# Kernel tuning notes

Measured on AMD Instinct MI355X. Metric: run time of the kernel, lower is better.

The kernel has to match this reference:

```python
import jax, jax.numpy as jnp
import numpy as np

FP8_MAX = 448.0  # max normal for float8_e4m3fn
BLOCK = 128


def setup_inputs() -> dict:
    key = jax.random.key(0)
    k1, k2, k3 = jax.random.split(key, 3)
    B, S, D_IN, D_OUT = 2, 2048, 4096, 8192
    x = jax.random.normal(k1, (B, S, D_IN), dtype=jnp.float32)
    # stored weight is fp8_e4m3fn; materialize as f32 values that are exactly fp8-representable
    w = jax.random.normal(k2, (D_OUT, D_IN), dtype=jnp.float32)
    weight = w.astype(jnp.float8_e4m3fn).astype(jnp.float32)
    # positive per-(128x128)-block dequant scales
    weight_scale_inv = (
        jax.random.uniform(k3, (D_OUT // BLOCK, D_IN // BLOCK), dtype=jnp.float32) * 0.05 + 0.005
    )
    return {"x": x, "weight": weight, "weight_scale_inv": weight_scale_inv}


def _quantize_per_token(x2d):
    # x2d: [M, K] -> fp8 values + [M, 1] f32 scale
    amax = jnp.clip(jnp.max(jnp.abs(x2d), axis=-1, keepdims=True), min=1e-12)
    x_scale = (amax / FP8_MAX).astype(jnp.float32)
    x_fp8 = (x2d / x_scale).astype(jnp.float8_e4m3fn)
    return x_fp8, x_scale


def _dequantize_weight(weight, weight_scale_inv):
    # weight: [O, K] (fp8-representable f32), scales: [O/B, K/B]
    O, K = weight.shape
    w_fp8 = weight.astype(jnp.float8_e4m3fn).astype(jnp.float32)
    wb = w_fp8.reshape(O // BLOCK, BLOCK, K // BLOCK, BLOCK)
    wb = wb * weight_scale_inv[:, None, :, None]
    return wb.reshape(O, K)


def reference(x, weight, weight_scale_inv):
    orig_shape = x.shape
    x2d = x.reshape(-1, orig_shape[-1])  # [M, K], M > 1 path
    x_fp8, x_scale = _quantize_per_token(x2d)
    # block-scaled fp8 GEMM: y[m,n] = x_scale[m] * sum_k x_fp8[m,k] * w_fp8[n,k] * s[n//B,k//B]
    w_deq = _dequantize_weight(weight, weight_scale_inv)  # [O, K]
    y = jnp.einsum("mk,ok->mo", x_fp8.astype(jnp.float32), w_deq) * x_scale
    return y.reshape(*orig_shape[:-1], weight.shape[0])
```

## Files before the change

### kernel.cpp

```cpp
#include <hip/hip_runtime.h>

typedef float f32x4  __attribute__((ext_vector_type(4)));
typedef float f32x16 __attribute__((ext_vector_type(16)));
typedef int   i32x4  __attribute__((ext_vector_type(4)));
typedef int   i32x8  __attribute__((ext_vector_type(8)));

#define AS1 __attribute__((address_space(1)))
#define AS3 __attribute__((address_space(3)))

__global__ __launch_bounds__(256) void quant_x_fp8_kernel(
    const float* __restrict__ x, unsigned char* __restrict__ x8,
    float* __restrict__ xs, int K) {
  int m = blockIdx.x;
  int t = threadIdx.x;
  const f32x4* src = (const f32x4*)(x + (size_t)m * K + t * 16);
  f32x4 v[4];
  float am = 0.0f;
#pragma unroll
  for (int i = 0; i < 4; ++i) {
    v[i] = src[i];
#pragma unroll
    for (int j = 0; j < 4; ++j) am = fmaxf(am, __builtin_fabsf(v[i][j]));
  }
#pragma unroll
  for (int off = 32; off >= 1; off >>= 1)
    am = fmaxf(am, __shfl_xor(am, off, 64));
  __shared__ float red[4];
  int wv = t >> 6, lane = t & 63;
  if (lane == 0) red[wv] = am;
  __syncthreads();
  am = fmaxf(fmaxf(red[0], red[1]), fmaxf(red[2], red[3]));
  am = fmaxf(am, 1e-12f);
  float sc = am / 448.0f;
  if (t == 0) xs[m] = sc;
  i32x4 out;
#pragma unroll
  for (int i = 0; i < 4; ++i) {
    float q0 = v[i][0] / sc, q1 = v[i][1] / sc;
    float q2 = v[i][2] / sc, q3 = v[i][3] / sc;
    int p = __builtin_amdgcn_cvt_pk_fp8_f32(q0, q1, 0, false);
    p = __builtin_amdgcn_cvt_pk_fp8_f32(q2, q3, p, true);
    out[i] = p;
  }
  *(i32x4*)(x8 + (size_t)m * K + t * 16) = out;
}

__global__ __launch_bounds__(256) void quant_w_fp8_kernel(
    const float* __restrict__ w, unsigned char* __restrict__ w8) {
  size_t idx = (size_t)blockIdx.x * 256 + threadIdx.x;
  const f32x4* src = (const f32x4*)w + idx * 4;
  i32x4 out;
#pragma unroll
  for (int i = 0; i < 4; ++i) {
    f32x4 v = src[i];
    int p = __builtin_amdgcn_cvt_pk_fp8_f32(v[0], v[1], 0, false);
    p = __builtin_amdgcn_cvt_pk_fp8_f32(v[2], v[3], p, true);
    out[i] = p;
  }
  ((i32x4*)w8)[idx] = out;
}

__global__ __launch_bounds__(256, 2) void gemm_mxfp8_kernel(
    const unsigned char* __restrict__ A8,
    const unsigned char* __restrict__ W8,
    const float* __restrict__ xs,
    const float* __restrict__ wsinv,
    float* __restrict__ Y,
    int M, int N, int K) {
  const int KB = K >> 7;

  int bid = blockIdx.x, nwg = gridDim.x;
  int wg = (bid & 7) * (nwg >> 3) + (bid >> 3);
  int mt = M >> 7;
  int bm = wg & (mt - 1);
  int bn = wg / mt;
  int m0 = bm << 7, n0 = bn << 7;

  __shared__ __align__(16) char lds[65536];

  const int tid = threadIdx.x, wv = tid >> 6, lane = tid & 63;
  const int wr = wv >> 1, wc = wv & 1;
  const int l31 = lane & 31, hi2 = lane >> 5;
  const int salt = l31 & 7;

  const int sL0 = ((hi2 * 2 + 0) ^ salt) << 4;
  const int sH0 = ((hi2 * 2 + 1) ^ salt) << 4;
  const int sL1 = ((4 + hi2 * 2 + 0) ^ salt) << 4;
  const int sH1 = ((4 + hi2 * 2 + 1) ^ salt) << 4;

  const int aRow = (wr * 64 + l31) * 128;
  const int bRow = (wc * 64 + l31) * 128;
  const int aL0 = aRow + sL0, aH0 = aRow + sH0;
  const int aL1 = aRow + sL1, aH1 = aRow + sH1;
  const int bL0 = bRow + sL0, bH0 = bRow + sH0;
  const int bL1 = bRow + sL1, bH1 = bRow + sH1;

  const int stgD = tid << 4;
  const int rIdx = tid >> 3;
  const int cSrc = ((tid & 7) ^ ((tid >> 3) & 7)) << 4;
  const size_t rowB = (size_t)K;
  const size_t g32 = 32 * rowB;
  const char* pA = (const char*)A8 + (size_t)(m0 + rIdx) * rowB + cSrc;
  const char* pB = (const char*)W8 + (size_t)(n0 + rIdx) * rowB + cSrc;

  const float* wsv = wsinv + (size_t)bn * KB;

  f32x16 acc[2][2];
#pragma unroll
  for (int i = 0; i < 2; ++i)
#pragma unroll
    for (int j = 0; j < 2; ++j) acc[i][j] = (f32x16)0.0f;

  i32x8 af[2], bf[2][2];

#define GL(SRC, DST)                                                           \
  __builtin_amdgcn_global_load_lds((const AS1 void*)(SRC), (AS3 void*)(DST),   \
                                   16, 0, 0)
#define STG(COND, SB, SRC)                                                     \
  if (COND) {                                                                  \
    const char* s_ = (SRC);                                                    \
    char* d_ = lds + (SB) + stgD;                                              \
    GL(s_, d_);                                                                \
    GL(s_ + g32, d_ + 4096);                                                   \
    GL(s_ + 2 * g32, d_ + 8192);                                               \
    GL(s_ + 3 * g32, d_ + 12288);                                              \
  }

#define RD_A(RB, MJ)                                                           \
  {                                                                            \
    const char* p_ = lds + (RB) + (MJ) * 4096;                                 \
    i32x4 lo0 = *(const i32x4*)(p_ + aL0);                                     \
    i32x4 hi0 = *(const i32x4*)(p_ + aH0);                                     \
    i32x4 lo1 = *(const i32x4*)(p_ + aL1);                                     \
    i32x4 hi1 = *(const i32x4*)(p_ + aH1);                                     \
    af[0] = __builtin_shufflevector(lo0, hi0, 0, 1, 2, 3, 4, 5, 6, 7);         \
    af[1] = __builtin_shufflevector(lo1, hi1, 0, 1, 2, 3, 4, 5, 6, 7);         \
  }
#define RD_B(RB)                                                               \
  _Pragma("unroll") for (int nj = 0; nj < 2; ++nj) {                           \
    const char* p_ = lds + (RB) + 16384 + nj * 4096;                           \
    i32x4 lo0 = *(const i32x4*)(p_ + bL0);                                     \
    i32x4 hi0 = *(const i32x4*)(p_ + bH0);                                     \
    i32x4 lo1 = *(const i32x4*)(p_ + bL1);                                     \
    i32x4 hi1 = *(const i32x4*)(p_ + bH1);                                     \
    bf[nj][0] = __builtin_shufflevector(lo0, hi0, 0, 1, 2, 3, 4, 5, 6, 7);     \
    bf[nj][1] = __builtin_shufflevector(lo1, hi1, 0, 1, 2, 3, 4, 5, 6, 7);     \
  }

#define MMFn(MJ, NJ, R_)                                                       \
  {                                                                            \
    _Pragma("unroll") for (int q = 0; q < 16; ++q)                             \
        acc[MJ][NJ][q] *= (R_);                                                \
    acc[MJ][NJ] = __builtin_amdgcn_mfma_scale_f32_32x32x64_f8f6f4(             \
        af[0], bf[NJ][0], acc[MJ][NJ], 0, 0, 0, 0x7f7f7f7f, 0, 0x7f7f7f7f);    \
    acc[MJ][NJ] = __builtin_amdgcn_mfma_scale_f32_32x32x64_f8f6f4(             \
        af[1], bf[NJ][1], acc[MJ][NJ], 0, 0, 0, 0x7f7f7f7f, 0, 0x7f7f7f7f);    \
  }

  STG(true, 0, pA);
  STG(true, 16384, pB);
  asm volatile("s_waitcnt vmcnt(0)" ::: "memory");
  __builtin_amdgcn_s_barrier();

  const char* pAs = pA + 128;
  const char* pBs = pB + 128;
  float sp_ = wsv[0];

#define TILE(T, RB, SB, G)                                                     \
  {                                                                            \
    float sc_ = wsv[(T)];                                                      \
    float r_ = sp_ / sc_;                                                      \
    RD_B(RB);                                                                  \
    RD_A(RB, 0);                                                               \
    STG(G, (SB), pAs);                                                         \
    STG(G, (SB) + 16384, pBs);                                                 \
    __builtin_amdgcn_s_setprio(1);                                             \
    MMFn(0, 0, r_);                                                            \
    MMFn(0, 1, r_);                                                            \
    __builtin_amdgcn_s_setprio(0);                                             \
    RD_A(RB, 1);                                                               \
    __builtin_amdgcn_s_setprio(1);                                             \
    MMFn(1, 0, r_);                                                            \
    MMFn(1, 1, r_);                                                            \
    __builtin_amdgcn_s_setprio(0);                                             \
    sp_ = sc_;                                                                 \
    asm volatile("s_waitcnt vmcnt(0)" ::: "memory");                           \
    __builtin_amdgcn_s_barrier();                                              \
    pAs += 128;                                                                \
    pBs += 128;                                                                \
  }

#pragma unroll 1
  for (int t = 0; t < KB; t += 2) {
    TILE(t, 0, 32768, true)
    TILE(t + 1, 32768, 0, (t + 2) < KB)
  }

#undef TILE
#undef MMFn
#undef RD_B
#undef RD_A
#undef STG
#undef GL

  const float sl_ = sp_;
#pragma unroll
  for (int mj = 0; mj < 2; ++mj)
#pragma unroll
    for (int nj = 0; nj < 2; ++nj) {
      int col = n0 + wc * 64 + nj * 32 + l31;
#pragma unroll
      for (int q = 0; q < 4; ++q) {
        int row0 = m0 + wr * 64 + mj * 32 + q * 8 + hi2 * 4;
        f32x4 sv = *(const f32x4*)(xs + row0);
#pragma unroll
        for (int j = 0; j < 4; ++j)
          Y[(size_t)(row0 + j) * N + col] = acc[mj][nj][q * 4 + j] * sv[j] * sl_;
      }
    }
}

extern "C" void kernel_launch(void* const* d_in, const int* in_sizes, int n_in,
                              void* d_out, int out_size, void* d_ws, size_t ws_size,
                              hipStream_t stream) {
  const float* x     = (const float*)d_in[0];
  const float* w     = (const float*)d_in[1];
  const float* wsinv = (const float*)d_in[2];
  float* y = (float*)d_out;

  const int K = 4096;
  const int M = in_sizes[0] / K;
  const int N = in_sizes[1] / K;

  unsigned char* x8 = (unsigned char*)d_ws;
  float* xs = (float*)((char*)d_ws + (size_t)M * K);
  unsigned char* w8 =
      (unsigned char*)d_ws + (size_t)M * K + (size_t)M * 4;

  quant_x_fp8_kernel<<<M, 256, 0, stream>>>(x, x8, xs, K);
  quant_w_fp8_kernel<<<(int)(((size_t)N * K / 16 + 255) / 256), 256, 0,
                       stream>>>(w, w8);

  dim3 grid((M / 128) * (N / 128));
  gemm_mxfp8_kernel<<<grid, 256, 0, stream>>>(x8, w8, xs, wsinv, y, M, N, K);
}
```

Before: 219.6 us.

## Load weight fragments directly from global into registers, bypassing LDS

B (weight) operands are no longer staged through LDS. Each lane loads its own MFMA fragments from global memory straight into registers, double-buffered across tiles (even/odd register sets). LDS shrinks to 32 KB, holding only the A tiles, which cuts LDS traffic and may allow more workgroups per CU. In exchange, weight data is no longer shared between waves with the same column (wr duplicates), so global/L2 traffic for B rises, register pressure goes up, and the per-lane loads are less coalesced.

After: 349.8 us. 1.59x slower.

```diff
diff --git a/kernel.cpp b/kernel.cpp
--- a/kernel.cpp
+++ b/kernel.cpp
@@ -76,7 +76,7 @@
   int bn = wg / mt;
   int m0 = bm << 7, n0 = bn << 7;
 
-  __shared__ __align__(16) char lds[65536];
+  __shared__ __align__(16) char lds[32768];
 
   const int tid = threadIdx.x, wv = tid >> 6, lane = tid & 63;
   const int wr = wv >> 1, wc = wv & 1;
@@ -89,19 +89,19 @@
   const int sH1 = ((4 + hi2 * 2 + 1) ^ salt) << 4;
 
   const int aRow = (wr * 64 + l31) * 128;
-  const int bRow = (wc * 64 + l31) * 128;
   const int aL0 = aRow + sL0, aH0 = aRow + sH0;
   const int aL1 = aRow + sL1, aH1 = aRow + sH1;
-  const int bL0 = bRow + sL0, bH0 = bRow + sH0;
-  const int bL1 = bRow + sL1, bH1 = bRow + sH1;
 
   const int stgD = tid << 4;
   const int rIdx = tid >> 3;
-  const int cSrc = ((tid & 7) ^ ((tid >> 3) & 7)) << 4;
+  const int cSrc = ((tid & 7) ^ (rIdx & 7)) << 4;
   const size_t rowB = (size_t)K;
   const size_t g32 = 32 * rowB;
   const char* pA = (const char*)A8 + (size_t)(m0 + rIdx) * rowB + cSrc;
-  const char* pB = (const char*)W8 + (size_t)(n0 + rIdx) * rowB + cSrc;
+
+  const char* pB0 = (const char*)W8 + (size_t)(n0 + wc * 64 + l31) * rowB +
+                    hi2 * 32;
+  const char* pB1 = pB0 + 32 * rowB;
 
   const float* wsv = wsinv + (size_t)bn * KB;
 
@@ -111,12 +111,12 @@
 #pragma unroll
     for (int j = 0; j < 2; ++j) acc[i][j] = (f32x16)0.0f;
 
-  i32x8 af[2], bf[2][2];
+  i32x8 af[2], bfE[2][2], bfO[2][2];
 
 #define GL(SRC, DST)                                                           \
   __builtin_amdgcn_global_load_lds((const AS1 void*)(SRC), (AS3 void*)(DST),   \
                                    16, 0, 0)
-#define STG(COND, SB, SRC)                                                     \
+#define STG_A(COND, SB, SRC)                                                   \
   if (COND) {                                                                  \
     const char* s_ = (SRC);                                                    \
     char* d_ = lds + (SB) + stgD;                                              \
@@ -136,71 +136,78 @@
     af[0] = __builtin_shufflevector(lo0, hi0, 0, 1, 2, 3, 4, 5, 6, 7);         \
     af[1] = __builtin_shufflevector(lo1, hi1, 0, 1, 2, 3, 4, 5, 6, 7);         \
   }
-#define RD_B(RB)                                                               \
-  _Pragma("unroll") for (int nj = 0; nj < 2; ++nj) {                           \
-    const char* p_ = lds + (RB) + 16384 + nj * 4096;                           \
-    i32x4 lo0 = *(const i32x4*)(p_ + bL0);                                     \
-    i32x4 hi0 = *(const i32x4*)(p_ + bH0);                                     \
-    i32x4 lo1 = *(const i32x4*)(p_ + bL1);                                     \
-    i32x4 hi1 = *(const i32x4*)(p_ + bH1);                                     \
-    bf[nj][0] = __builtin_shufflevector(lo0, hi0, 0, 1, 2, 3, 4, 5, 6, 7);     \
-    bf[nj][1] = __builtin_shufflevector(lo1, hi1, 0, 1, 2, 3, 4, 5, 6, 7);     \
-  }
-
-#define MMFn(MJ, NJ, R_)                                                       \
+
+#define LDB(COND, DST)                                                         \
+  if (COND) {                                                                  \
+    i32x4 l0 = *(const i32x4*)(pB0);                                           \
+    i32x4 h0 = *(const i32x4*)(pB0 + 16);                                      \
+    i32x4 l1 = *(const i32x4*)(pB0 + 64);                                      \
+    i32x4 h1 = *(const i32x4*)(pB0 + 80);                                      \
+    DST[0][0] = __builtin_shufflevector(l0, h0, 0, 1, 2, 3, 4, 5, 6, 7);       \
+    DST[0][1] = __builtin_shufflevector(l1, h1, 0, 1, 2, 3, 4, 5, 6, 7);       \
+    l0 = *(const i32x4*)(pB1);                                                 \
+    h0 = *(const i32x4*)(pB1 + 16);                                            \
+    l1 = *(const i32x4*)(pB1 + 64);                                            \
+    h1 = *(const i32x4*)(pB1 + 80);                                            \
+    DST[1][0] = __builtin_shufflevector(l0, h0, 0, 1, 2, 3, 4, 5, 6, 7);       \
+    DST[1][1] = __builtin_shufflevector(l1, h1, 0, 1, 2, 3, 4, 5, 6, 7);       \
+  }
+
+#define MMFn(MJ, NJ, R_, BF)                                                   \
   {                                                                            \
     _Pragma("unroll") for (int q = 0; q < 16; ++q)                             \
         acc[MJ][NJ][q] *= (R_);                                                \
     acc[MJ][NJ] = __builtin_amdgcn_mfma_scale_f32_32x32x64_f8f6f4(             \
-        af[0], bf[NJ][0], acc[MJ][NJ], 0, 0, 0, 0x7f7f7f7f, 0, 0x7f7f7f7f);    \
+        af[0], BF[NJ][0], acc[MJ][NJ], 0, 0, 0, 0x7f7f7f7f, 0, 0x7f7f7f7f);    \
     acc[MJ][NJ] = __builtin_amdgcn_mfma_scale_f32_32x32x64_f8f6f4(             \
-        af[1], bf[NJ][1], acc[MJ][NJ], 0, 0, 0, 0x7f7f7f7f, 0, 0x7f7f7f7f);    \
-  }
-
-  STG(true, 0, pA);
-  STG(true, 16384, pB);
+        af[1], BF[NJ][1], acc[MJ][NJ], 0, 0, 0, 0x7f7f7f7f, 0, 0x7f7f7f7f);    \
+  }
+
+  STG_A(true, 0, pA);
+  LDB(true, bfE);
+  pB0 += 128;
+  pB1 += 128;
   asm volatile("s_waitcnt vmcnt(0)" ::: "memory");
   __builtin_amdgcn_s_barrier();
 
   const char* pAs = pA + 128;
-  const char* pBs = pB + 128;
   float sp_ = wsv[0];
 
-#define TILE(T, RB, SB, G)                                                     \
+#define TILE(T, RB, SB, G, BFC, BFN)                                           \
   {                                                                            \
     float sc_ = wsv[(T)];                                                      \
     float r_ = sp_ / sc_;                                                      \
-    RD_B(RB);                                                                  \
+    sp_ = sc_;                                                                 \
+    LDB(G, BFN);                                                               \
+    STG_A(G, (SB), pAs);                                                       \
     RD_A(RB, 0);                                                               \
-    STG(G, (SB), pAs);                                                         \
-    STG(G, (SB) + 16384, pBs);                                                 \
     __builtin_amdgcn_s_setprio(1);                                             \
-    MMFn(0, 0, r_);                                                            \
-    MMFn(0, 1, r_);                                                            \
+    MMFn(0, 0, r_, BFC);                                                       \
+    MMFn(0, 1, r_, BFC);                                                       \
     __builtin_amdgcn_s_setprio(0);                                             \
     RD_A(RB, 1);                                                               \
     __builtin_amdgcn_s_setprio(1);                                             \
-    MMFn(1, 0, r_);                                                            \
-    MMFn(1, 1, r_);                                                            \
+    MMFn(1, 0, r_, BFC);                                                       \
+    MMFn(1, 1, r_, BFC);                                                       \
     __builtin_amdgcn_s_setprio(0);                                             \
-    sp_ = sc_;                                                                 \
     asm volatile("s_waitcnt vmcnt(0)" ::: "memory");                           \
     __builtin_amdgcn_s_barrier();                                              \
     pAs += 128;                                                                \
-    pBs += 128;                                                                \
+    pB0 += 128;                                                                \
+    pB1 += 128;                                                                \
   }
 
 #pragma unroll 1
   for (int t = 0; t < KB; t += 2) {
-    TILE(t, 0, 32768, true)
-    TILE(t + 1, 32768, 0, (t + 2) < KB)
+    TILE(t, 0, 16384, true, bfE, bfO)
+    TILE(t + 1, 16384, 0, (t + 2) < KB, bfO, bfE)
   }
 
 #undef TILE
 #undef MMFn
-#undef RD_B
+#undef LDB
 #undef RD_A
-#undef STG
+#undef STG_A
 #undef GL
 
   const float sl_ = sp_;
```

## Triple-buffer 64-wide K half-tiles with register double-buffered fragments

Applied to the files above, without the earlier changes.

Restructures the GEMM main loop to stage 64-byte K slices into three 16KB LDS buffers instead of two 32KB buffers for 128-wide tiles. A and B fragments are double-buffered in registers (even/odd sets), so LDS reads for the next slice overlap the MFMAs of the current one. Global loads stay in flight across iterations through partial vmcnt waits. The loop trip count is hardcoded for K=4096 (32 scale blocks), and LDS use drops from 64KB to 48KB, which may allow better occupancy.

New measurement: 243.3 us. +10.8%, slower.

```diff
diff --git a/kernel.cpp b/kernel.cpp
--- a/kernel.cpp
+++ b/kernel.cpp
@@ -76,32 +76,33 @@
   int bn = wg / mt;
   int m0 = bm << 7, n0 = bn << 7;
 
-  __shared__ __align__(16) char lds[65536];
+  __shared__ __align__(16) char lds[49152];
 
   const int tid = threadIdx.x, wv = tid >> 6, lane = tid & 63;
   const int wr = wv >> 1, wc = wv & 1;
   const int l31 = lane & 31, hi2 = lane >> 5;
-  const int salt = l31 & 7;
-
-  const int sL0 = ((hi2 * 2 + 0) ^ salt) << 4;
-  const int sH0 = ((hi2 * 2 + 1) ^ salt) << 4;
-  const int sL1 = ((4 + hi2 * 2 + 0) ^ salt) << 4;
-  const int sH1 = ((4 + hi2 * 2 + 1) ^ salt) << 4;
-
-  const int aRow = (wr * 64 + l31) * 128;
-  const int bRow = (wc * 64 + l31) * 128;
-  const int aL0 = aRow + sL0, aH0 = aRow + sH0;
-  const int aL1 = aRow + sL1, aH1 = aRow + sH1;
-  const int bL0 = bRow + sL0, bH0 = bRow + sH0;
-  const int bL1 = bRow + sL1, bH1 = bRow + sH1;
+
+  const int lineB = (l31 >> 1) * 128;
+  const int par4 = (l31 & 1) << 2;
+  const int xr = (l31 >> 1) & 7;
+  const int s0 = 2 * hi2, s1 = 2 * hi2 + 1;
+  const int slotL = ((par4 | s0) ^ xr) << 4;
+  const int slotH = ((par4 | s1) ^ xr) << 4;
+  const int aL0 = wr * 4096 + lineB + slotL;
+  const int aH0 = wr * 4096 + lineB + slotH;
+  const int aL1 = aL0 + 2048, aH1 = aH0 + 2048;
+  const int bL0 = 8192 + wc * 4096 + lineB + slotL;
+  const int bH0 = 8192 + wc * 4096 + lineB + slotH;
+  const int bL1 = bL0 + 2048, bH1 = bH0 + 2048;
 
   const int stgD = tid << 4;
-  const int rIdx = tid >> 3;
-  const int cSrc = ((tid & 7) ^ ((tid >> 3) & 7)) << 4;
+  const int inv = (tid & 7) ^ ((tid >> 3) & 7);
+  const int rLoc = 2 * (tid >> 3) + (inv >> 2);
+  const int cSrc = (inv & 3) << 4;
   const size_t rowB = (size_t)K;
-  const size_t g32 = 32 * rowB;
-  const char* pA = (const char*)A8 + (size_t)(m0 + rIdx) * rowB + cSrc;
-  const char* pB = (const char*)W8 + (size_t)(n0 + rIdx) * rowB + cSrc;
+  const size_t g64r = 64 * rowB;
+  const char* pA = (const char*)A8 + (size_t)(m0 + rLoc) * rowB + cSrc;
+  const char* pB = (const char*)W8 + (size_t)(n0 + rLoc) * rowB + cSrc;
 
   const float* wsv = wsinv + (size_t)bn * KB;
 
@@ -111,96 +112,125 @@
 #pragma unroll
     for (int j = 0; j < 2; ++j) acc[i][j] = (f32x16)0.0f;
 
-  i32x8 af[2], bf[2][2];
+  i32x8 afE[2], bfE[2], afO[2], bfO[2];
 
 #define GL(SRC, DST)                                                           \
   __builtin_amdgcn_global_load_lds((const AS1 void*)(SRC), (AS3 void*)(DST),   \
                                    16, 0, 0)
-#define STG(COND, SB, SRC)                                                     \
+#define STG_P(COND, SB, SRC)                                                   \
   if (COND) {                                                                  \
     const char* s_ = (SRC);                                                    \
     char* d_ = lds + (SB) + stgD;                                              \
     GL(s_, d_);                                                                \
-    GL(s_ + g32, d_ + 4096);                                                   \
-    GL(s_ + 2 * g32, d_ + 8192);                                               \
-    GL(s_ + 3 * g32, d_ + 12288);                                              \
-  }
-
-#define RD_A(RB, MJ)                                                           \
+    GL(s_ + g64r, d_ + 4096);                                                  \
+  }
+#define STG(COND, BUF)                                                         \
+  STG_P(COND, (BUF), pAs)                                                      \
+  STG_P(COND, (BUF) + 8192, pBs)
+
+#define RD_F(BUF, AF, BF)                                                      \
   {                                                                            \
-    const char* p_ = lds + (RB) + (MJ) * 4096;                                 \
-    i32x4 lo0 = *(const i32x4*)(p_ + aL0);                                     \
-    i32x4 hi0 = *(const i32x4*)(p_ + aH0);                                     \
-    i32x4 lo1 = *(const i32x4*)(p_ + aL1);                                     \
-    i32x4 hi1 = *(const i32x4*)(p_ + aH1);                                     \
-    af[0] = __builtin_shufflevector(lo0, hi0, 0, 1, 2, 3, 4, 5, 6, 7);         \
-    af[1] = __builtin_shufflevector(lo1, hi1, 0, 1, 2, 3, 4, 5, 6, 7);         \
-  }
-#define RD_B(RB)                                                               \
+    const char* q_ = lds + (BUF);                                              \
+    i32x4 t0_ = *(const i32x4*)(q_ + aL0);                                     \
+    i32x4 t1_ = *(const i32x4*)(q_ + aH0);                                     \
+    AF[0] = __builtin_shufflevector(t0_, t1_, 0, 1, 2, 3, 4, 5, 6, 7);         \
+    t0_ = *(const i32x4*)(q_ + aL1);                                           \
+    t1_ = *(const i32x4*)(q_ + aH1);                                           \
+    AF[1] = __builtin_shufflevector(t0_, t1_, 0, 1, 2, 3, 4, 5, 6, 7);         \
+    t0_ = *(const i32x4*)(q_ + bL0);                                           \
+    t1_ = *(const i32x4*)(q_ + bH0);                                           \
+    BF[0] = __builtin_shufflevector(t0_, t1_, 0, 1, 2, 3, 4, 5, 6, 7);         \
+    t0_ = *(const i32x4*)(q_ + bL1);                                           \
+    t1_ = *(const i32x4*)(q_ + bH1);                                           \
+    BF[1] = __builtin_shufflevector(t0_, t1_, 0, 1, 2, 3, 4, 5, 6, 7);         \
+  }
+
+#define MME(AF, BF, R_)                                                        \
+  _Pragma("unroll") for (int mj = 0; mj < 2; ++mj)                             \
   _Pragma("unroll") for (int nj = 0; nj < 2; ++nj) {                           \
-    const char* p_ = lds + (RB) + 16384 + nj * 4096;                           \
-    i32x4 lo0 = *(const i32x4*)(p_ + bL0);                                     \
-    i32x4 hi0 = *(const i32x4*)(p_ + bH0);                                     \
-    i32x4 lo1 = *(const i32x4*)(p_ + bL1);                                     \
-    i32x4 hi1 = *(const i32x4*)(p_ + bH1);                                     \
-    bf[nj][0] = __builtin_shufflevector(lo0, hi0, 0, 1, 2, 3, 4, 5, 6, 7);     \
-    bf[nj][1] = __builtin_shufflevector(lo1, hi1, 0, 1, 2, 3, 4, 5, 6, 7);     \
-  }
-
-#define MMFn(MJ, NJ, R_)                                                       \
+    _Pragma("unroll") for (int q = 0; q < 16; ++q)                             \
+        acc[mj][nj][q] *= (R_);                                                \
+    acc[mj][nj] = __builtin_amdgcn_mfma_scale_f32_32x32x64_f8f6f4(             \
+        AF[mj], BF[nj], acc[mj][nj], 0, 0, 0, 0x7f7f7f7f, 0, 0x7f7f7f7f);      \
+  }
+#define MMD(AF, BF)                                                            \
+  _Pragma("unroll") for (int mj = 0; mj < 2; ++mj)                             \
+  _Pragma("unroll") for (int nj = 0; nj < 2; ++nj)                             \
+    acc[mj][nj] = __builtin_amdgcn_mfma_scale_f32_32x32x64_f8f6f4(             \
+        AF[mj], BF[nj], acc[mj][nj], 0, 0, 0, 0x7f7f7f7f, 0, 0x7f7f7f7f);
+
+#define BODY_E(SC_, RDB, STB, G, VM)                                           \
   {                                                                            \
-    _Pragma("unroll") for (int q = 0; q < 16; ++q)                             \
-        acc[MJ][NJ][q] *= (R_);                                                \
-    acc[MJ][NJ] = __builtin_amdgcn_mfma_scale_f32_32x32x64_f8f6f4(             \
-        af[0], bf[NJ][0], acc[MJ][NJ], 0, 0, 0, 0x7f7f7f7f, 0, 0x7f7f7f7f);    \
-    acc[MJ][NJ] = __builtin_amdgcn_mfma_scale_f32_32x32x64_f8f6f4(             \
-        af[1], bf[NJ][1], acc[MJ][NJ], 0, 0, 0, 0x7f7f7f7f, 0, 0x7f7f7f7f);    \
-  }
-
-  STG(true, 0, pA);
-  STG(true, 16384, pB);
-  asm volatile("s_waitcnt vmcnt(0)" ::: "memory");
+    float sc_ = (SC_);                                                         \
+    float r_ = sp_ / sc_;                                                      \
+    sp_ = sc_;                                                                 \
+    RD_F(RDB, afO, bfO);                                                       \
+    STG(G, STB);                                                               \
+    __builtin_amdgcn_s_setprio(1);                                             \
+    MME(afE, bfE, r_);                                                         \
+    __builtin_amdgcn_s_setprio(0);                                             \
+    asm volatile("s_waitcnt lgkmcnt(0)" ::: "memory");                         \
+    asm volatile("s_waitcnt " VM ::: "memory");                                \
+    __builtin_amdgcn_s_barrier();                                              \
+    pAs += 64;                                                                 \
+    pBs += 64;                                                                 \
+  }
+#define BODY_O(RDB, STB, G, VM)                                                \
+  {                                                                            \
+    RD_F(RDB, afE, bfE);                                                       \
+    STG(G, STB);                                                               \
+    __builtin_amdgcn_s_setprio(1);                                             \
+    MMD(afO, bfO);                                                             \
+    __builtin_amdgcn_s_setprio(0);                                             \
+    asm volatile("s_waitcnt lgkmcnt(0)" ::: "memory");                         \
+    asm volatile("s_waitcnt " VM ::: "memory");                                \
+    __builtin_amdgcn_s_barrier();                                              \
+    pAs += 64;                                                                 \
+    pBs += 64;                                                                 \
+  }
+
+  {
+    const char* pAs = pA;
+    const char* pBs = pB;
+    STG(true, 0);
+    pAs += 64; pBs += 64;
+    STG(true, 16384);
+    pAs += 64; pBs += 64;
+    STG(true, 32768);
+  }
+  asm volatile("s_waitcnt vmcnt(4)" ::: "memory");
   __builtin_amdgcn_s_barrier();
-
-  const char* pAs = pA + 128;
-  const char* pBs = pB + 128;
+  RD_F(0, afE, bfE);
+  asm volatile("s_waitcnt lgkmcnt(0)" ::: "memory");
+  __builtin_amdgcn_s_barrier();
+
+  const char* pAs = pA + 192;
+  const char* pBs = pB + 192;
   float sp_ = wsv[0];
 
-#define TILE(T, RB, SB, G)                                                     \
-  {                                                                            \
-    float sc_ = wsv[(T)];                                                      \
-    float r_ = sp_ / sc_;                                                      \
-    RD_B(RB);                                                                  \
-    RD_A(RB, 0);                                                               \
-    STG(G, (SB), pAs);                                                         \
-    STG(G, (SB) + 16384, pBs);                                                 \
-    __builtin_amdgcn_s_setprio(1);                                             \
-    MMFn(0, 0, r_);                                                            \
-    MMFn(0, 1, r_);                                                            \
-    __builtin_amdgcn_s_setprio(0);                                             \
-    RD_A(RB, 1);                                                               \
-    __builtin_amdgcn_s_setprio(1);                                             \
-    MMFn(1, 0, r_);                                                            \
-    MMFn(1, 1, r_);                                                            \
-    __builtin_amdgcn_s_setprio(0);                                             \
-    sp_ = sc_;                                                                 \
-    asm volatile("s_waitcnt vmcnt(0)" ::: "memory");                           \
-    __builtin_amdgcn_s_barrier();                                              \
-    pAs += 128;                                                                \
-    pBs += 128;                                                                \
-  }
-
 #pragma unroll 1
-  for (int t = 0; t < KB; t += 2) {
-    TILE(t, 0, 32768, true)
-    TILE(t + 1, 32768, 0, (t + 2) < KB)
-  }
-
-#undef TILE
-#undef MMFn
-#undef RD_B
-#undef RD_A
+  for (int t0 = 0; t0 < 30; t0 += 3) {
+    BODY_E(wsv[t0],     16384, 0,     true, "vmcnt(4)")
+    BODY_O(             32768, 16384, true, "vmcnt(4)")
+    BODY_E(wsv[t0 + 1], 0,     32768, true, "vmcnt(4)")
+    BODY_O(             16384, 0,     true, "vmcnt(4)")
+    BODY_E(wsv[t0 + 2], 32768, 16384, true, "vmcnt(4)")
+    BODY_O(             0,     32768, true, "vmcnt(4)")
+  }
+  BODY_E(wsv[30], 16384, 0,     true,  "vmcnt(4)")
+  BODY_O(         32768, 0,     false, "vmcnt(0)")
+  BODY_E(wsv[31], 0,     0,     false, "vmcnt(0)")
+  __builtin_amdgcn_s_setprio(1);
+  MMD(afO, bfO);
+  __builtin_amdgcn_s_setprio(0);
+
+#undef BODY_O
+#undef BODY_E
+#undef MMD
+#undef MME
+#undef RD_F
 #undef STG
+#undef STG_P
 #undef GL
 
   const float sl_ = sp_;
```
